# Optimization experiments

Measured on AMD Instinct MI355X. Metric: run time of the kernel, lower is better.

The kernel has to match this reference:

```python
import jax, jax.numpy as jnp
import numpy as np

B, S, H = 2, 2048, 1024
NH = 16
HD = H // NH


def setup_inputs() -> dict:
    key = jax.random.key(0)
    ks = jax.random.split(key, 9)
    std = 1.0 / np.sqrt(H)
    inp = {"x": jax.random.normal(ks[0], (B, S, H), dtype=jnp.float32)}
    names = ["Wq", "Wk", "Wv", "Wo"]
    for i, n in enumerate(names):
        inp[n] = jax.random.uniform(ks[1 + i], (H, H), dtype=jnp.float32, minval=-std, maxval=std)
        inp["b" + n[1:]] = jax.random.uniform(ks[5 + i], (H,), dtype=jnp.float32, minval=-std, maxval=std)
    return inp


def reference(x, Wq, Wk, Wv, Wo, bq, bk, bv, bo):
    scale = HD ** -0.5
    # projections: torch Linear is x @ W.T + b
    def proj(W, b):
        y = jnp.einsum('bsh,oh->bso', x, W) + b
        return y.reshape(B, S, NH, HD).transpose(0, 2, 1, 3)  # [B, NH, S, HD]
    Q = proj(Wq, bq)
    K = proj(Wk, bk)
    V = proj(Wv, bv)
    scores = jnp.einsum('bhqd,bhkd->bhqk', Q, K) * scale  # [B, NH, S, S]
    attn = jax.nn.softmax(scores, axis=-1)
    ctx = jnp.einsum('bhqk,bhkd->bhqd', attn, V)
    ctx = ctx.transpose(0, 2, 1, 3).reshape(B, S, H)
    out = jnp.einsum('bsh,oh->bso', ctx, Wo) + bo
    avg_attention = attn.mean(axis=1).mean(axis=1)  # [B, S] (mean over heads, then query dim)
    return out, avg_attention
```

## Files before the change

kernel.cpp:

```cpp
#include <hip/hip_runtime.h>
#include <hip/hip_bf16.h>

#define B_  2
#define S_  2048
#define H_  1024
#define NH_ 16
#define HD_ 64
#define NTOK (B_*S_)

typedef __attribute__((ext_vector_type(8))) short bf16x8;
typedef __attribute__((ext_vector_type(4))) float f32x4;

#define SC2 0.18033688011112042f

static __device__ __forceinline__ ushort f2bf(float f) {
    __hip_bfloat16 h = __float2bfloat16(f);
    return *reinterpret_cast<ushort*>(&h);
}
static __device__ __forceinline__ uint cvt_pk_bf16(float lo, float hi) {
    uint r;
    asm("v_cvt_pk_bf16_f32 %0, %1, %2" : "=v"(r) : "v"(lo), "v"(hi));
    return r;
}

static __device__ __forceinline__ void gload_lds16(const void* g, void* l) {
    __builtin_amdgcn_global_load_lds(
        (const __attribute__((address_space(1))) void*)g,
        (__attribute__((address_space(3))) void*)l,
        16, 0, 0);
}

struct PrepArgs {
    const float* src[5];
    ushort*      dst[5];
    float*       zero;
};

static __device__ __forceinline__ void conv8(const float* __restrict__ s,
                                             ushort* __restrict__ d, int i)
{
    const float4 a = reinterpret_cast<const float4*>(s)[2*i + 0];
    const float4 b = reinterpret_cast<const float4*>(s)[2*i + 1];
    ushort u[8];
    u[0] = f2bf(a.x); u[1] = f2bf(a.y); u[2] = f2bf(a.z); u[3] = f2bf(a.w);
    u[4] = f2bf(b.x); u[5] = f2bf(b.y); u[6] = f2bf(b.z); u[7] = f2bf(b.w);
    reinterpret_cast<uint4*>(d)[i] = *reinterpret_cast<uint4*>(u);
}

__global__ __launch_bounds__(256) void prep(PrepArgs a)
{
    int bid = blockIdx.x;
    const int t = threadIdx.x;
    if (bid < 2048) {
        conv8(a.src[0], a.dst[0], bid*256 + t);
        return;
    }
    bid -= 2048;
    if (bid < 2048) {
        const int wi = 1 + (bid >> 9);
        const int i  = (bid & 511)*256 + t;
        conv8(a.src[wi], a.dst[wi], i);
        return;
    }
    bid -= 2048;
    const int i = bid*256 + t;
    if (i < NTOK) a.zero[i] = 0.f;
}

__global__ __launch_bounds__(256) void transpose_v(
    const ushort* __restrict__ Vb, ushort* __restrict__ Vt)
{
    __shared__ ushort T[64][72];
    const int t  = threadIdx.x;
    const int b  = blockIdx.z;
    const int h  = blockIdx.y;
    const int s0 = blockIdx.x * 64;
    const int r  = t >> 2;
    const int c0 = (t & 3) * 16;

    const ushort* src = Vb + (size_t)(b*S_ + s0 + r)*H_ + h*HD_ + c0;
    *reinterpret_cast<uint4*>(&T[r][c0])     = *reinterpret_cast<const uint4*>(src);
    *reinterpret_cast<uint4*>(&T[r][c0 + 8]) = *reinterpret_cast<const uint4*>(src + 8);
    __syncthreads();

    const int d = r;
    ushort tmp[16];
#pragma unroll
    for (int k = 0; k < 16; ++k) tmp[k] = T[c0 + k][d];
    ushort* dst = Vt + ((size_t)((b*NH_ + h)*HD_ + d))*S_ + s0 + c0;
    *reinterpret_cast<uint4*>(dst)     = *reinterpret_cast<uint4*>(&tmp[0]);
    *reinterpret_cast<uint4*>(dst + 8) = *reinterpret_cast<uint4*>(&tmp[8]);
}

struct GemmArgs {
    const ushort* W[3];
    const float*  bias[3];
    void*         Y[3];
    float         scale[3];
};

__global__ __launch_bounds__(256) void gemm_qkv(
    const ushort* __restrict__ A, GemmArgs args, int M, int N, int K)
{
    constexpr int MREP = 4;
    constexpr int BM = MREP * 32;
    __shared__ __align__(16) ushort As[BM * 64];
    __shared__ __align__(16) ushort Bs[128 * 64];

    const int z = blockIdx.z;
    const ushort* __restrict__ W   = args.W[z];
    const float*  __restrict__ bia = args.bias[z];
    const float sc = args.scale[z];

    const int t  = threadIdx.x;
    const int w  = t >> 6;
    const int l  = t & 63;
    const int lq = l >> 4;
    const int ln = l & 15;
    const int wr = w >> 1;
    const int wc = w & 1;
    const int m0 = blockIdx.x * BM;
    const int n0 = blockIdx.y * 128;
    const int srow = l >> 3;
    const int scol = (l & 7) * 8;

    f32x4 acc[MREP][4];
#pragma unroll
    for (int m = 0; m < MREP; ++m)
#pragma unroll
        for (int n = 0; n < 4; ++n) acc[m][n] = f32x4{0.f, 0.f, 0.f, 0.f};

    for (int k0 = 0; k0 < K; k0 += 64) {
        __syncthreads();
#pragma unroll
        for (int i = 0; i < BM/32; ++i) {
            const int rb = i*32 + w*8;
            gload_lds16(A + (size_t)(m0 + rb + srow)*K + k0 + scol, &As[rb*64]);
        }
#pragma unroll
        for (int i = 0; i < 4; ++i) {
            const int rb = i*32 + w*8;
            gload_lds16(W + (size_t)(n0 + rb + srow)*K + k0 + scol, &Bs[rb*64]);
        }
        __syncthreads();
#pragma unroll
        for (int ks = 0; ks < 2; ++ks) {
            bf16x8 bfr[4];
#pragma unroll
            for (int n = 0; n < 4; ++n)
                bfr[n] = *reinterpret_cast<const bf16x8*>(&Bs[(wc*64 + n*16 + ln)*64 + ks*32 + lq*8]);
#pragma unroll
            for (int m = 0; m < MREP; ++m) {
                const bf16x8 afr = *reinterpret_cast<const bf16x8*>(&As[(wr*MREP*16 + m*16 + ln)*64 + ks*32 + lq*8]);
#pragma unroll
                for (int n = 0; n < 4; ++n)
                    acc[m][n] = __builtin_amdgcn_mfma_f32_16x16x32_bf16(afr, bfr[n], acc[m][n], 0, 0, 0);
            }
        }
    }

    float bv[4];
#pragma unroll
    for (int n = 0; n < 4; ++n) bv[n] = bia[n0 + wc*64 + n*16 + ln];

    ushort* Y = (ushort*)args.Y[z];
#pragma unroll
    for (int m = 0; m < MREP; ++m) {
#pragma unroll
        for (int r = 0; r < 4; ++r) {
            const size_t row = (size_t)(m0 + wr*MREP*16 + m*16 + lq*4 + r);
#pragma unroll
            for (int n = 0; n < 4; ++n) {
                const int col = n0 + wc*64 + n*16 + ln;
                Y[row*N + col] = f2bf((acc[m][n][r] + bv[n]) * sc);
            }
        }
    }
}

__global__ __launch_bounds__(256) void attn_pv(
    const ushort* __restrict__ Qb, const ushort* __restrict__ Kb,
    const ushort* __restrict__ Vtg, ushort* __restrict__ ctx,
    float* __restrict__ il2_g)
{
    __shared__ __align__(16) ushort Ks0[64*64];
    __shared__ __align__(16) ushort Ks1[64*64];
    __shared__ __align__(16) ushort Vs0[64*64];
    __shared__ __align__(16) ushort Vs1[64*64];
    __shared__ __align__(16) ushort Ps[4][16*64];

    const int t  = threadIdx.x;
    const int w  = t >> 6;
    const int l  = t & 63;
    const int lq = l >> 4;
    const int ln = l & 15;
    const int b  = blockIdx.z;
    const int h  = blockIdx.y;
    const int q0 = blockIdx.x * 64;
    const int ln7 = ln & 7;

    bf16x8 qf[2];
    {
        const ushort* qrow = Qb + ((size_t)(b*S_ + q0 + w*16 + ln))*H_ + h*HD_ + lq*8;
        qf[0] = *reinterpret_cast<const bf16x8*>(qrow);
        qf[1] = *reinterpret_cast<const bf16x8*>(qrow + 32);
    }

    bf16x8 onesb;
#pragma unroll
    for (int j = 0; j < 8; ++j) onesb[j] = (short)0x3F80;

    size_t koff[2], voff[2];
    int    dsto[2];
#pragma unroll
    for (int i = 0; i < 2; ++i) {
        const int chunk = i*256 + t;
        const int row   = chunk >> 3;
        const int c8    = (chunk & 7) ^ (row & 7);
        koff[i] = (size_t)(b*S_ + row)*H_ + h*HD_ + c8*8;
        voff[i] = ((size_t)((b*NH_ + h)*HD_ + row))*S_ + c8*8;
        dsto[i] = chunk*8;
    }

    f32x4 lsacc = f32x4{0.f, 0.f, 0.f, 0.f};
    f32x4 oacc[4];
#pragma unroll
    for (int nt = 0; nt < 4; ++nt) oacc[nt] = f32x4{0.f, 0.f, 0.f, 0.f};

    auto tile_body = [&](const ushort* __restrict__ ksb, const ushort* __restrict__ vsb,
                         int pre_kt, bool do_pre,
                         ushort* __restrict__ kdst, ushort* __restrict__ vdst) {
        if (do_pre) {
#pragma unroll
            for (int i = 0; i < 2; ++i) {
                gload_lds16(Kb + koff[i] + (size_t)pre_kt*H_, &kdst[dsto[i]]);
                gload_lds16(Vtg + voff[i] + pre_kt, &vdst[dsto[i]]);
            }
        }

        f32x4 sacc[4];
#pragma unroll
        for (int nt = 0; nt < 4; ++nt) sacc[nt] = f32x4{0.f, 0.f, 0.f, 0.f};
#pragma unroll
        for (int ks = 0; ks < 2; ++ks) {
            bf16x8 kb[4];
#pragma unroll
            for (int nt = 0; nt < 4; ++nt)
                kb[nt] = *reinterpret_cast<const bf16x8*>(
                    &ksb[(nt*16 + ln)*64 + (((ks*4 + lq) ^ ln7) * 8)]);
#pragma unroll
            for (int nt = 0; nt < 4; ++nt)
                sacc[nt] = __builtin_amdgcn_mfma_f32_16x16x32_bf16(
                    kb[nt], qf[ks], sacc[nt], 0, 0, 0);
        }

#pragma unroll
        for (int nt = 0; nt < 4; ++nt) {
            const float e0 = exp2f(sacc[nt][0]);
            const float e1 = exp2f(sacc[nt][1]);
            const float e2 = exp2f(sacc[nt][2]);
            const float e3 = exp2f(sacc[nt][3]);
            uint2 pk;
            pk.x = cvt_pk_bf16(e0, e1);
            pk.y = cvt_pk_bf16(e2, e3);
            const int wch = (nt*2 + (lq >> 1)) ^ ln7;
            *reinterpret_cast<uint2*>(&Ps[w][ln*64 + wch*8 + (lq & 1)*4]) = pk;
        }

#pragma unroll
        for (int ks = 0; ks < 2; ++ks) {
            const bf16x8 pa = *reinterpret_cast<const bf16x8*>(
                &Ps[w][ln*64 + (((ks*4 + lq) ^ ln7) * 8)]);
            lsacc = __builtin_amdgcn_mfma_f32_16x16x32_bf16(pa, onesb, lsacc, 0, 0, 0);
#pragma unroll
            for (int nt = 0; nt < 4; ++nt) {
                const bf16x8 vb8 = *reinterpret_cast<const bf16x8*>(
                    &vsb[(nt*16 + ln)*64 + (((ks*4 + lq) ^ ln7) * 8)]);
                oacc[nt] = __builtin_amdgcn_mfma_f32_16x16x32_bf16(
                    pa, vb8, oacc[nt], 0, 0, 0);
            }
        }

        __syncthreads();
    };

#pragma unroll
    for (int i = 0; i < 2; ++i) {
        gload_lds16(Kb + koff[i], &Ks0[dsto[i]]);
        gload_lds16(Vtg + voff[i], &Vs0[dsto[i]]);
    }
    __syncthreads();

    for (int kt = 0; kt < S_; kt += 128) {
        tile_body(Ks0, Vs0, kt + 64, true, Ks1, Vs1);
        tile_body(Ks1, Vs1, kt + 128, kt + 128 < S_, Ks0, Vs0);
    }

    float ivr[4];
#pragma unroll
    for (int r = 0; r < 4; ++r) ivr[r] = 1.f / lsacc[r];

    if (ln == 0) {
        float4 o;
        o.x = -__log2f(lsacc[0]);
        o.y = -__log2f(lsacc[1]);
        o.z = -__log2f(lsacc[2]);
        o.w = -__log2f(lsacc[3]);
        *reinterpret_cast<float4*>(
            il2_g + (size_t)(b*NH_ + h)*S_ + q0 + w*16 + lq*4) = o;
    }

    ushort* crow = ctx + ((size_t)(b*S_ + q0 + w*16 + lq*4))*H_ + h*HD_ + ln;
#pragma unroll
    for (int r = 0; r < 4; ++r)
#pragma unroll
        for (int nt = 0; nt < 4; ++nt)
            crow[(size_t)r*H_ + nt*16] = f2bf(oacc[nt][r] * ivr[r]);
}

struct FusedArgs {
    const ushort* Qb; const ushort* Kb;
    const float*  il2; float* colsum;
    const ushort* A;  const ushort* W;
    const float*  bias; float* Y;
};

__global__ __launch_bounds__(256) void colsum_outproj(FusedArgs fa)
{
    __shared__ __align__(16) char smem[32768];
    const int id = blockIdx.x;
    const int t  = threadIdx.x;
    const int w  = t >> 6;
    const int l  = t & 63;
    const int lq = l >> 4;
    const int ln = l & 15;
    const int ln7 = ln & 7;

    if (id < 1024) {
        ushort* KsT = (ushort*)smem;
        ushort* Qs0 = (ushort*)(smem + 8192);
        ushort* Qs1 = (ushort*)(smem + 16384);
        float*  iv  = (float*)(smem + 24576);

        const int k0 = (id & 31) * 64;
        const int h  = (id >> 5) & 15;
        const int b  = id >> 9;
        const int bh = b*NH_ + h;

        int crow_[2], cc8[2], dsto[2];
#pragma unroll
        for (int i = 0; i < 2; ++i) {
            const int chunk = i*256 + t;
            crow_[i] = chunk >> 3;
            cc8[i]   = (chunk & 7) ^ (crow_[i] & 7);
            dsto[i]  = chunk*8;
        }

#pragma unroll
        for (int i = 0; i < 2; ++i) {
            gload_lds16(fa.Kb + (size_t)(b*S_ + k0 + crow_[i])*H_ + h*HD_ + cc8[i]*8, &KsT[dsto[i]]);
            gload_lds16(fa.il2 + (size_t)bh*S_ + (i*256 + t)*4, &iv[(i*256 + t)*4]);
            gload_lds16(fa.Qb + (size_t)(b*S_ + crow_[i])*H_ + h*HD_ + cc8[i]*8, &Qs0[dsto[i]]);
        }
        __syncthreads();

        bf16x8 kf[2];
#pragma unroll
        for (int ks = 0; ks < 2; ++ks)
            kf[ks] = *reinterpret_cast<const bf16x8*>(
                &KsT[(w*16 + ln)*64 + (((ks*4 + lq) ^ ln7) * 8)]);

        float cs4[4] = {0.f, 0.f, 0.f, 0.f};

        for (int qt = 0; qt < S_; qt += 128) {
#pragma unroll
            for (int i = 0; i < 2; ++i)
                gload_lds16(fa.Qb + (size_t)(b*S_ + qt + 64 + crow_[i])*H_ + h*HD_ + cc8[i]*8,
                            &Qs1[dsto[i]]);
#pragma unroll
            for (int c = 0; c < 4; ++c) {
                f32x4 sacc = f32x4{0.f, 0.f, 0.f, 0.f};
#pragma unroll
                for (int ks = 0; ks < 2; ++ks) {
                    const bf16x8 af = *reinterpret_cast<const bf16x8*>(
                        &Qs0[(c*16 + ln)*64 + (((ks*4 + lq) ^ ln7) * 8)]);
                    sacc = __builtin_amdgcn_mfma_f32_16x16x32_bf16(af, kf[ks], sacc, 0, 0, 0);
                }
                const f32x4 iv4 = *reinterpret_cast<const f32x4*>(&iv[qt + c*16 + lq*4]);
#pragma unroll
                for (int r = 0; r < 4; ++r)
                    cs4[r] += exp2f(sacc[r] + iv4[r]);
            }
            __syncthreads();

            if (qt + 128 < S_) {
#pragma unroll
                for (int i = 0; i < 2; ++i)
                    gload_lds16(fa.Qb + (size_t)(b*S_ + qt + 128 + crow_[i])*H_ + h*HD_ + cc8[i]*8,
                                &Qs0[dsto[i]]);
            }
#pragma unroll
            for (int c = 0; c < 4; ++c) {
                f32x4 sacc = f32x4{0.f, 0.f, 0.f, 0.f};
#pragma unroll
                for (int ks = 0; ks < 2; ++ks) {
                    const bf16x8 af = *reinterpret_cast<const bf16x8*>(
                        &Qs1[(c*16 + ln)*64 + (((ks*4 + lq) ^ ln7) * 8)]);
                    sacc = __builtin_amdgcn_mfma_f32_16x16x32_bf16(af, kf[ks], sacc, 0, 0, 0);
                }
                const f32x4 iv4 = *reinterpret_cast<const f32x4*>(&iv[qt + 64 + c*16 + lq*4]);
#pragma unroll
                for (int r = 0; r < 4; ++r)
                    cs4[r] += exp2f(sacc[r] + iv4[r]);
            }
            __syncthreads();
        }

        float cs = (cs4[0] + cs4[1]) + (cs4[2] + cs4[3]);
        cs += __shfl_xor(cs, 16);
        cs += __shfl_xor(cs, 32);
        if (l < 16)
            atomicAdd(&fa.colsum[(size_t)b*S_ + k0 + w*16 + l], cs);
    } else {
        ushort* As = (ushort*)smem;
        ushort* Bs = (ushort*)(smem + 8192);

        const int g  = id - 1024;
        const int m0 = (g & 63) * 64;
        const int n0 = (g >> 6) * 128;
        const int wr = w >> 1;
        const int wc = w & 1;
        const int srow = l >> 3;
        const int scol = (l & 7) * 8;

        f32x4 acc[2][4];
#pragma unroll
        for (int m = 0; m < 2; ++m)
#pragma unroll
            for (int n = 0; n < 4; ++n) acc[m][n] = f32x4{0.f, 0.f, 0.f, 0.f};

        for (int k0 = 0; k0 < H_; k0 += 64) {
            __syncthreads();
#pragma unroll
            for (int i = 0; i < 2; ++i) {
                const int rb = i*32 + w*8;
                gload_lds16(fa.A + (size_t)(m0 + rb + srow)*H_ + k0 + scol, &As[rb*64]);
            }
#pragma unroll
            for (int i = 0; i < 4; ++i) {
                const int rb = i*32 + w*8;
                gload_lds16(fa.W + (size_t)(n0 + rb + srow)*H_ + k0 + scol, &Bs[rb*64]);
            }
            __syncthreads();
#pragma unroll
            for (int ks = 0; ks < 2; ++ks) {
                bf16x8 bfr[4];
#pragma unroll
                for (int n = 0; n < 4; ++n)
                    bfr[n] = *reinterpret_cast<const bf16x8*>(&Bs[(wc*64 + n*16 + ln)*64 + ks*32 + lq*8]);
#pragma unroll
                for (int m = 0; m < 2; ++m) {
                    const bf16x8 afr = *reinterpret_cast<const bf16x8*>(&As[(wr*32 + m*16 + ln)*64 + ks*32 + lq*8]);
#pragma unroll
                    for (int n = 0; n < 4; ++n)
                        acc[m][n] = __builtin_amdgcn_mfma_f32_16x16x32_bf16(afr, bfr[n], acc[m][n], 0, 0, 0);
                }
            }
        }

        float bv[4];
#pragma unroll
        for (int n = 0; n < 4; ++n) bv[n] = fa.bias[n0 + wc*64 + n*16 + ln];

#pragma unroll
        for (int m = 0; m < 2; ++m) {
#pragma unroll
            for (int r = 0; r < 4; ++r) {
                const size_t row = (size_t)(m0 + wr*32 + m*16 + lq*4 + r);
#pragma unroll
                for (int n = 0; n < 4; ++n) {
                    const int col = n0 + wc*64 + n*16 + ln;
                    fa.Y[row*H_ + col] = acc[m][n][r] + bv[n];
                }
            }
        }
    }
}

__global__ void avg_write(const float* __restrict__ colsum, float* __restrict__ out, float inv)
{
    const int i = blockIdx.x * 256 + threadIdx.x;
    if (i < NTOK) out[i] = colsum[i] * inv;
}

extern "C" void kernel_launch(void* const* d_in, const int* in_sizes, int n_in,
                              void* d_out, int out_size, void* d_ws, size_t ws_size,
                              hipStream_t stream)
{
    const float* x  = (const float*)d_in[0];
    const float* Wq = (const float*)d_in[1];
    const float* bq = (const float*)d_in[2];
    const float* Wk = (const float*)d_in[3];
    const float* bk = (const float*)d_in[4];
    const float* Wv = (const float*)d_in[5];
    const float* bv = (const float*)d_in[6];
    const float* Wo = (const float*)d_in[7];
    const float* bo = (const float*)d_in[8];

    float* out     = (float*)d_out;
    float* avg_out = out + (size_t)NTOK * H_;

    char* ws = (char*)d_ws;
    const size_t mat  = (size_t)NTOK * H_ * sizeof(ushort);
    const size_t wmat = (size_t)H_ * H_ * sizeof(ushort);
    ushort* xb   = (ushort*)(ws);
    ushort* Qb   = (ushort*)(ws + mat);
    ushort* Kb   = (ushort*)(ws + 2*mat);
    ushort* Vb   = (ushort*)(ws + 3*mat);
    ushort* Vtg  = (ushort*)(ws + 4*mat);
    ushort* Wqb  = (ushort*)(ws + 5*mat);
    ushort* Wkb  = (ushort*)(ws + 5*mat + wmat);
    ushort* Wvb  = (ushort*)(ws + 5*mat + 2*wmat);
    ushort* Wob  = (ushort*)(ws + 5*mat + 3*wmat);
    float*  colsum = (float*)(ws + 5*mat + 4*wmat);
    float*  il2    = (float*)(ws + 5*mat + 4*wmat + 64*1024);
    ushort* ctxb = xb;

    const dim3 blk(256);

    {
        PrepArgs pa;
        pa.src[0] = x;  pa.dst[0] = xb;
        pa.src[1] = Wq; pa.dst[1] = Wqb;
        pa.src[2] = Wk; pa.dst[2] = Wkb;
        pa.src[3] = Wv; pa.dst[3] = Wvb;
        pa.src[4] = Wo; pa.dst[4] = Wob;
        pa.zero = colsum;
        prep<<<dim3(4112), blk, 0, stream>>>(pa);
    }

    {
        GemmArgs ga;
        ga.W[0] = Wqb; ga.W[1] = Wkb; ga.W[2] = Wvb;
        ga.bias[0] = bq; ga.bias[1] = bk; ga.bias[2] = bv;
        ga.Y[0] = Qb; ga.Y[1] = Kb; ga.Y[2] = Vb;
        ga.scale[0] = SC2; ga.scale[1] = 1.f; ga.scale[2] = 1.f;
        gemm_qkv<<<dim3(NTOK/128, H_/128, 3), blk, 0, stream>>>(xb, ga, NTOK, H_, H_);
    }

    transpose_v<<<dim3(S_/64, NH_, B_), blk, 0, stream>>>(Vb, Vtg);

    attn_pv<<<dim3(S_/64, NH_, B_), blk, 0, stream>>>(Qb, Kb, Vtg, ctxb, il2);

    {
        FusedArgs fa;
        fa.Qb = Qb; fa.Kb = Kb; fa.il2 = il2; fa.colsum = colsum;
        fa.A = ctxb; fa.W = Wob; fa.bias = bo; fa.Y = out;
        colsum_outproj<<<dim3(1536), blk, 0, stream>>>(fa);
    }

    avg_write<<<dim3((NTOK + 255)/256), blk, 0, stream>>>(colsum, avg_out, 1.f/((float)NH_ * (float)S_));
}
```

Before: 183.0 us.

## Remap attention block order for L2 locality and drop the avg_write kernel

Both attention kernels now use a 1D grid whose block index interleaves 8 (batch,head) pairs across consecutive blocks. The intent is that blocks resident on the GPU at the same time share heads and hit the same K/V in cache, with the goal of better L2 or Infinity Cache reuse. The column-sum atomics now write pre-scaled values directly into the avg output, which prep zeroes, so the separate avg_write launch goes away. The first MFMA in each k-step now takes a zero accumulator, which removes some zero-initialisation work.

Result: no change. 180.5 us (-1.4%).

```diff
diff --git a/kernel.cpp b/kernel.cpp
--- a/kernel.cpp
+++ b/kernel.cpp
@@ -12,6 +12,7 @@
 typedef __attribute__((ext_vector_type(4))) float f32x4;
 
 #define SC2 0.18033688011112042f
+#define AVGINV (1.f/((float)NH_*(float)S_))
 
 static __device__ __forceinline__ ushort f2bf(float f) {
     __hip_bfloat16 h = __float2bfloat16(f);
@@ -189,14 +190,18 @@
     __shared__ __align__(16) ushort Vs1[64*64];
     __shared__ __align__(16) ushort Ps[4][16*64];
 
+    const int id = blockIdx.x;
+    const int qt_ = (id >> 3) & 31;
+    const int bh  = (id & 7) + ((id >> 8) << 3);
+    const int b   = bh >> 4;
+    const int h   = bh & 15;
+    const int q0  = qt_ * 64;
+
     const int t  = threadIdx.x;
     const int w  = t >> 6;
     const int l  = t & 63;
     const int lq = l >> 4;
     const int ln = l & 15;
-    const int b  = blockIdx.z;
-    const int h  = blockIdx.y;
-    const int q0 = blockIdx.x * 64;
     const int ln7 = ln & 7;
 
     bf16x8 qf[2];
@@ -209,6 +214,8 @@
     bf16x8 onesb;
 #pragma unroll
     for (int j = 0; j < 8; ++j) onesb[j] = (short)0x3F80;
+
+    const f32x4 ZED = f32x4{0.f, 0.f, 0.f, 0.f};
 
     size_t koff[2], voff[2];
     int    dsto[2];
@@ -222,10 +229,10 @@
         dsto[i] = chunk*8;
     }
 
-    f32x4 lsacc = f32x4{0.f, 0.f, 0.f, 0.f};
+    f32x4 lsacc = ZED;
     f32x4 oacc[4];
 #pragma unroll
-    for (int nt = 0; nt < 4; ++nt) oacc[nt] = f32x4{0.f, 0.f, 0.f, 0.f};
+    for (int nt = 0; nt < 4; ++nt) oacc[nt] = ZED;
 
     auto tile_body = [&](const ushort* __restrict__ ksb, const ushort* __restrict__ vsb,
                          int pre_kt, bool do_pre,
@@ -239,19 +246,27 @@
         }
 
         f32x4 sacc[4];
-#pragma unroll
-        for (int nt = 0; nt < 4; ++nt) sacc[nt] = f32x4{0.f, 0.f, 0.f, 0.f};
-#pragma unroll
-        for (int ks = 0; ks < 2; ++ks) {
+        {
             bf16x8 kb[4];
 #pragma unroll
             for (int nt = 0; nt < 4; ++nt)
                 kb[nt] = *reinterpret_cast<const bf16x8*>(
-                    &ksb[(nt*16 + ln)*64 + (((ks*4 + lq) ^ ln7) * 8)]);
+                    &ksb[(nt*16 + ln)*64 + ((lq ^ ln7) * 8)]);
 #pragma unroll
             for (int nt = 0; nt < 4; ++nt)
                 sacc[nt] = __builtin_amdgcn_mfma_f32_16x16x32_bf16(
-                    kb[nt], qf[ks], sacc[nt], 0, 0, 0);
+                    kb[nt], qf[0], ZED, 0, 0, 0);
+        }
+        {
+            bf16x8 kb[4];
+#pragma unroll
+            for (int nt = 0; nt < 4; ++nt)
+                kb[nt] = *reinterpret_cast<const bf16x8*>(
+                    &ksb[(nt*16 + ln)*64 + (((4 + lq) ^ ln7) * 8)]);
+#pragma unroll
+            for (int nt = 0; nt < 4; ++nt)
+                sacc[nt] = __builtin_amdgcn_mfma_f32_16x16x32_bf16(
+                    kb[nt], qf[1], sacc[nt], 0, 0, 0);
         }
 
 #pragma unroll
@@ -320,7 +335,7 @@
 
 struct FusedArgs {
     const ushort* Qb; const ushort* Kb;
-    const float*  il2; float* colsum;
+    const float*  il2; float* avg_out;
     const ushort* A;  const ushort* W;
     const float*  bias; float* Y;
 };
@@ -335,6 +350,7 @@
     const int lq = l >> 4;
     const int ln = l & 15;
     const int ln7 = ln & 7;
+    const f32x4 ZED = f32x4{0.f, 0.f, 0.f, 0.f};
 
     if (id < 1024) {
         ushort* KsT = (ushort*)smem;
@@ -342,10 +358,11 @@
         ushort* Qs1 = (ushort*)(smem + 16384);
         float*  iv  = (float*)(smem + 24576);
 
-        const int k0 = (id & 31) * 64;
-        const int h  = (id >> 5) & 15;
-        const int b  = id >> 9;
-        const int bh = b*NH_ + h;
+        const int kt_ = (id >> 3) & 31;
+        const int bh  = (id & 7) + ((id >> 8) << 3);
+        const int b   = bh >> 4;
+        const int h   = bh & 15;
+        const int k0  = kt_ * 64;
 
         int crow_[2], cc8[2], dsto[2];
 #pragma unroll
@@ -379,13 +396,12 @@
                             &Qs1[dsto[i]]);
 #pragma unroll
             for (int c = 0; c < 4; ++c) {
-                f32x4 sacc = f32x4{0.f, 0.f, 0.f, 0.f};
-#pragma unroll
-                for (int ks = 0; ks < 2; ++ks) {
-                    const bf16x8 af = *reinterpret_cast<const bf16x8*>(
-                        &Qs0[(c*16 + ln)*64 + (((ks*4 + lq) ^ ln7) * 8)]);
-                    sacc = __builtin_amdgcn_mfma_f32_16x16x32_bf16(af, kf[ks], sacc, 0, 0, 0);
-                }
+                const bf16x8 a0 = *reinterpret_cast<const bf16x8*>(
+                    &Qs0[(c*16 + ln)*64 + ((lq ^ ln7) * 8)]);
+                const bf16x8 a1 = *reinterpret_cast<const bf16x8*>(
+                    &Qs0[(c*16 + ln)*64 + (((4 + lq) ^ ln7) * 8)]);
+                f32x4 sacc = __builtin_amdgcn_mfma_f32_16x16x32_bf16(a0, kf[0], ZED, 0, 0, 0);
+                sacc = __builtin_amdgcn_mfma_f32_16x16x32_bf16(a1, kf[1], sacc, 0, 0, 0);
                 const f32x4 iv4 = *reinterpret_cast<const f32x4*>(&iv[qt + c*16 + lq*4]);
 #pragma unroll
                 for (int r = 0; r < 4; ++r)
@@ -401,13 +417,12 @@
             }
 #pragma unroll
             for (int c = 0; c < 4; ++c) {
-                f32x4 sacc = f32x4{0.f, 0.f, 0.f, 0.f};
-#pragma unroll
-                for (int ks = 0; ks < 2; ++ks) {
-                    const bf16x8 af = *reinterpret_cast<const bf16x8*>(
-                        &Qs1[(c*16 + ln)*64 + (((ks*4 + lq) ^ ln7) * 8)]);
-                    sacc = __builtin_amdgcn_mfma_f32_16x16x32_bf16(af, kf[ks], sacc, 0, 0, 0);
-                }
+                const bf16x8 a0 = *reinterpret_cast<const bf16x8*>(
+                    &Qs1[(c*16 + ln)*64 + ((lq ^ ln7) * 8)]);
+                const bf16x8 a1 = *reinterpret_cast<const bf16x8*>(
+                    &Qs1[(c*16 + ln)*64 + (((4 + lq) ^ ln7) * 8)]);
+                f32x4 sacc = __builtin_amdgcn_mfma_f32_16x16x32_bf16(a0, kf[0], ZED, 0, 0, 0);
+                sacc = __builtin_amdgcn_mfma_f32_16x16x32_bf16(a1, kf[1], sacc, 0, 0, 0);
                 const f32x4 iv4 = *reinterpret_cast<const f32x4*>(&iv[qt + 64 + c*16 + lq*4]);
 #pragma unroll
                 for (int r = 0; r < 4; ++r)
@@ -420,7 +435,7 @@
         cs += __shfl_xor(cs, 16);
         cs += __shfl_xor(cs, 32);
         if (l < 16)
-            atomicAdd(&fa.colsum[(size_t)b*S_ + k0 + w*16 + l], cs);
+            atomicAdd(&fa.avg_out[(size_t)b*S_ + k0 + w*16 + l], cs * AVGINV);
     } else {
         ushort* As = (ushort*)smem;
         ushort* Bs = (ushort*)(smem + 8192);
@@ -437,7 +452,7 @@
 #pragma unroll
         for (int m = 0; m < 2; ++m)
 #pragma unroll
-            for (int n = 0; n < 4; ++n) acc[m][n] = f32x4{0.f, 0.f, 0.f, 0.f};
+            for (int n = 0; n < 4; ++n) acc[m][n] = ZED;
 
         for (int k0 = 0; k0 < H_; k0 += 64) {
             __syncthreads();
@@ -485,12 +500,6 @@
             }
         }
     }
-}
-
-__global__ void avg_write(const float* __restrict__ colsum, float* __restrict__ out, float inv)
-{
-    const int i = blockIdx.x * 256 + threadIdx.x;
-    if (i < NTOK) out[i] = colsum[i] * inv;
 }
 
 extern "C" void kernel_launch(void* const* d_in, const int* in_sizes, int n_in,
@@ -522,8 +531,7 @@
     ushort* Wkb  = (ushort*)(ws + 5*mat + wmat);
     ushort* Wvb  = (ushort*)(ws + 5*mat + 2*wmat);
     ushort* Wob  = (ushort*)(ws + 5*mat + 3*wmat);
-    float*  colsum = (float*)(ws + 5*mat + 4*wmat);
-    float*  il2    = (float*)(ws + 5*mat + 4*wmat + 64*1024);
+    float*  il2  = (float*)(ws + 5*mat + 4*wmat);
     ushort* ctxb = xb;
 
     const dim3 blk(256);
@@ -535,7 +543,7 @@
         pa.src[2] = Wk; pa.dst[2] = Wkb;
         pa.src[3] = Wv; pa.dst[3] = Wvb;
         pa.src[4] = Wo; pa.dst[4] = Wob;
-        pa.zero = colsum;
+        pa.zero = avg_out;
         prep<<<dim3(4112), blk, 0, stream>>>(pa);
     }
 
@@ -550,14 +558,12 @@
 
     transpose_v<<<dim3(S_/64, NH_, B_), blk, 0, stream>>>(Vb, Vtg);
 
-    attn_pv<<<dim3(S_/64, NH_, B_), blk, 0, stream>>>(Qb, Kb, Vtg, ctxb, il2);
+    attn_pv<<<dim3(1024), blk, 0, stream>>>(Qb, Kb, Vtg, ctxb, il2);
 
     {
         FusedArgs fa;
-        fa.Qb = Qb; fa.Kb = Kb; fa.il2 = il2; fa.colsum = colsum;
+        fa.Qb = Qb; fa.Kb = Kb; fa.il2 = il2; fa.avg_out = avg_out;
         fa.A = ctxb; fa.W = Wob; fa.bias = bo; fa.Y = out;
         colsum_outproj<<<dim3(1536), blk, 0, stream>>>(fa);
     }
-
-    avg_write<<<dim3((NTOK + 255)/256), blk, 0, stream>>>(colsum, avg_out, 1.f/((float)NH_ * (float)S_));
-}
+}
```
